# Performance work log

Measured on AMD Instinct MI355X. Metric: run time of the kernel, lower is better.

The kernel has to match this reference:

```python
import jax, jax.numpy as jnp
import numpy as np

M, N, C, D = 2, 8, 1024, 256  # n_routers, num_adapters, channel_dim, down_sample_size
B, S = 32, 512


def setup_inputs() -> dict:
    key = jax.random.key(0)
    k1, k2, k3, k4, k5 = jax.random.split(key, 5)
    x = jax.random.normal(k1, (B, S, C), dtype=jnp.float32)
    expert_index = jax.random.randint(k2, (M, B), 0, N, dtype=jnp.int32)
    down_w = jax.random.normal(k3, (M, N, C, D), dtype=jnp.float32) * 0.01
    down_b = jax.random.normal(k4, (M, N, D), dtype=jnp.float32) * 0.01
    up_w = jax.random.normal(k5, (M, N, D, C), dtype=jnp.float32) * 0.01
    return {"x": x, "expert_index": expert_index, "down_w": down_w,
            "down_b": down_b, "up_w": up_w}


def reference(x, expert_index, down_w, down_b, up_w):
    # Gather per-(router, batch-element) adapter weights along the adapter axis.
    idx = expert_index  # [M, B]
    bw_down = jnp.take_along_axis(down_w, idx[:, :, None, None], axis=1)  # [M, B, C, D]
    bb_down = jnp.take_along_axis(down_b, idx[:, :, None], axis=1)        # [M, B, D]
    bw_up = jnp.take_along_axis(up_w, idx[:, :, None, None], axis=1)      # [M, B, D, C]
    # z = swish(x @ W_down + b_down)  -> [M, B, S, D]
    z = jnp.einsum('bsc,mbcd->mbsd', x, bw_down) + bb_down[:, :, None, :]
    z = jax.nn.silu(z)
    # u = z @ W_up -> [M, B, S, C]
    u = jnp.einsum('mbsd,mbdc->mbsc', z, bw_up)
    return u
```

## Files before the change

### kernel.cpp

```cpp
#include <hip/hip_runtime.h>
#include <stdint.h>

typedef unsigned short u16;
typedef __bf16 bf16x8 __attribute__((ext_vector_type(8)));
typedef float f32x4 __attribute__((ext_vector_type(4)));

#define MM 2
#define NN 8
#define CC 1024
#define DD 256
#define BB 32
#define SS 512

__device__ __forceinline__ u16 f2bf(float f) {
  uint32_t u = __float_as_uint(f);
  u += 0x7FFFu + ((u >> 16) & 1u);
  return (u16)(u >> 16);
}

__device__ __forceinline__ uint32_t pack2(float a, float b) {
  return (uint32_t)f2bf(a) | ((uint32_t)f2bf(b) << 16);
}

__device__ __forceinline__ void async16(const void* g, void* l) {
  __builtin_amdgcn_global_load_lds(
      (const __attribute__((address_space(1))) uint32_t*)g,
      (__attribute__((address_space(3))) uint32_t*)l, 16, 0, 0);
}

__global__ __launch_bounds__(256) void prep_w(
    const float* __restrict__ dw, u16* __restrict__ wdT,
    const float* __restrict__ uw, u16* __restrict__ wuT,
    const float* __restrict__ x, u16* __restrict__ xb) {
  int bid = blockIdx.x;
  if (bid >= 4096) {
    const int t = bid - 4096;
    const float4* in4 = reinterpret_cast<const float4*>(x) + (size_t)t * 2048;
    uint2* out2 = reinterpret_cast<uint2*>(xb) + (size_t)t * 2048;
    const int tx = threadIdx.x;
#pragma unroll
    for (int k = 0; k < 8; ++k) {
      float4 v = in4[k * 256 + tx];
      out2[k * 256 + tx] = make_uint2(pack2(v.x, v.y), pack2(v.z, v.w));
    }
    return;
  }
  __shared__ float tile[64][33];
  const float* src; u16* dst; int K, N, tk, tn;
  if (bid < 2048) {
    K = CC; N = DD;
    const int slab = bid >> 7, t = bid & 127;
    tk = t >> 3; tn = t & 7;
    src = dw + (size_t)slab * K * N;
    dst = wdT + (size_t)slab * K * N;
  } else {
    bid -= 2048;
    K = DD; N = CC;
    const int slab = bid >> 7, t = bid & 127;
    tk = t >> 5; tn = t & 31;
    src = uw + (size_t)slab * K * N;
    dst = wuT + (size_t)slab * K * N;
  }
  const int k0 = tk * 64, n0 = tn * 32;
  const int tx = threadIdx.x & 31, ty = threadIdx.x >> 5;
#pragma unroll
  for (int i = 0; i < 64; i += 8)
    tile[ty + i][tx] = src[(size_t)(k0 + ty + i) * N + n0 + tx];
  __syncthreads();
  uint32_t* dst32 = reinterpret_cast<uint32_t*>(dst);
#pragma unroll
  for (int i = 0; i < 32; i += 8) {
    const int nr = ty + i;
    dst32[((size_t)(n0 + nr) * K + k0) / 2 + tx] =
        pack2(tile[2 * tx][nr], tile[2 * tx + 1][nr]);
  }
}

__global__ __launch_bounds__(512, 2) void fused_adapter(
    const u16* __restrict__ xb, const u16* __restrict__ wdT,
    const u16* __restrict__ wuT, const float* __restrict__ db,
    const int* __restrict__ eidx, float* __restrict__ out) {
  __shared__ __align__(16) u16 smA[2][128 * 64];
  __shared__ __align__(16) u16 smB[2][256 * 64];
  __shared__ __align__(16) u16 zl[8 * 128 * 32];

  const int id = blockIdx.x;
  const int xcd = id & 7;
  const int j5 = id >> 3;
  const int stile = j5 >> 3;
  const int m = (j5 >> 2) & 1;
  const int b = xcd * 4 + (j5 & 3);
  const int pair = m * BB + b;
  const int e = eidx[pair];
  const int s0 = stile * 128;

  const int tid = threadIdx.x;
  const int lane = tid & 63;
  const int wave = tid >> 6;
  const int quad = lane >> 4;
  const int l16 = lane & 15;
  const int fx = (l16 >> 1) & 3;
  const int fxr = l16 & 7;

  const int wr = (wave >> 2) * 64;
  const int wc = (wave & 3) * 64;

  const u16* Bd = wdT + (size_t)(m * NN + e) * DD * CC;
  const u16* Bu = wuT + (size_t)(m * NN + e) * CC * DD;

  const float* bias_p = db + (size_t)(m * NN + e) * DD;
  float biasr[4];
#pragma unroll
  for (int j = 0; j < 4; ++j) biasr[j] = bias_p[wc + j * 16 + l16];

  const int r_l = lane >> 3;
  const int sx = (lane & 7) ^ r_l;

  const u16* gA = xb + ((size_t)b * SS + s0 + wave * 16 + r_l) * CC + sx * 8;
  const u16* gBd = Bd + (size_t)(wave * 32 + r_l) * CC + sx * 8;
  const u16* gBu = Bu + (size_t)(wave * 32 + r_l) * DD + sx * 8;

  f32x4 acc[4][4];
#pragma unroll
  for (int i = 0; i < 4; ++i)
#pragma unroll
    for (int j = 0; j < 4; ++j) acc[i][j] = (f32x4){0.f, 0.f, 0.f, 0.f};

#pragma unroll
  for (int s = 0; s < 2; ++s)
    async16(gA + (size_t)(s * 8) * CC, &smA[0][(wave * 16 + s * 8) * 64]);
#pragma unroll
  for (int s = 0; s < 4; ++s)
    async16(gBd + (size_t)(s * 8) * CC, &smB[0][(wave * 32 + s * 8) * 64]);
  asm volatile("s_waitcnt vmcnt(0) lgkmcnt(0)" ::: "memory");
  __builtin_amdgcn_s_barrier();

  for (int kk = 0; kk < 16; ++kk) {
    const int cur = kk & 1, nxt = cur ^ 1;
    if (kk < 15) {
      const int ko = (kk + 1) * 64;
#pragma unroll
      for (int s = 0; s < 2; ++s)
        async16(gA + (size_t)(s * 8) * CC + ko, &smA[nxt][(wave * 16 + s * 8) * 64]);
#pragma unroll
      for (int s = 0; s < 4; ++s)
        async16(gBd + (size_t)(s * 8) * CC + ko, &smB[nxt][(wave * 32 + s * 8) * 64]);
    } else {
#pragma unroll
      for (int s = 0; s < 4; ++s)
        async16(gBu + (size_t)(s * 8) * DD, &smB[nxt][(wave * 32 + s * 8) * 64]);
    }
#pragma unroll
    for (int h = 0; h < 2; ++h) {
      bf16x8 af[4], bfr[4];
#pragma unroll
      for (int i = 0; i < 4; ++i)
        af[i] = *reinterpret_cast<const bf16x8*>(
            &smA[cur][(wr + i * 16 + l16) * 64 + ((h * 4 + quad) ^ fxr) * 8]);
#pragma unroll
      for (int j = 0; j < 4; ++j)
        bfr[j] = *reinterpret_cast<const bf16x8*>(
            &smB[cur][(wc + j * 16 + l16) * 64 + ((h * 4 + quad) ^ fxr) * 8]);
      __builtin_amdgcn_s_setprio(1);
#pragma unroll
      for (int i = 0; i < 4; ++i)
#pragma unroll
        for (int j = 0; j < 4; ++j)
          acc[i][j] = __builtin_amdgcn_mfma_f32_16x16x32_bf16(af[i], bfr[j], acc[i][j], 0, 0, 0);
      __builtin_amdgcn_s_setprio(0);
    }
    asm volatile("s_waitcnt vmcnt(0) lgkmcnt(0)" ::: "memory");
    __builtin_amdgcn_s_barrier();
  }

#pragma unroll
  for (int j = 0; j < 4; ++j) {
    const int d = wc + j * 16 + l16;
    const int kt = d >> 5;
    const int kl = d & 31;
    const int slot0 = kl >> 3;
    const int kin = kl & 7;
#pragma unroll
    for (int i = 0; i < 4; ++i) {
      const int zr = wr + i * 16 + quad * 4;
#pragma unroll
      for (int r = 0; r < 4; ++r) {
        const int row = zr + r;
        float v = acc[i][j][r] + biasr[j];
        v = v / (1.f + __expf(-v));
        zl[kt * 4096 + row * 32 + ((slot0 ^ ((row >> 1) & 3)) * 8) + kin] = f2bf(v);
      }
    }
  }
  asm volatile("s_waitcnt lgkmcnt(0)" ::: "memory");
  __builtin_amdgcn_s_barrier();

  float* ob = out + ((size_t)pair * SS + s0) * CC;

  for (int g = 0; g < 16; ++g) {
    const int cur2 = g & 1, nxt2 = cur2 ^ 1;
    const int ct = g >> 2;
    const int it2 = g & 3;
    if (g < 15) {
      const int g2 = g + 1;
      const size_t ro = (size_t)(g2 >> 2) * 256 * DD + (g2 & 3) * 64;
#pragma unroll
      for (int s = 0; s < 4; ++s)
        async16(gBu + ro + (size_t)(s * 8) * DD, &smB[nxt2][(wave * 32 + s * 8) * 64]);
    }
    if (it2 == 0) {
#pragma unroll
      for (int i = 0; i < 4; ++i)
#pragma unroll
        for (int j = 0; j < 4; ++j) acc[i][j] = (f32x4){0.f, 0.f, 0.f, 0.f};
    }
#pragma unroll
    for (int h = 0; h < 2; ++h) {
      bf16x8 af[4], bfr[4];
#pragma unroll
      for (int i = 0; i < 4; ++i)
        af[i] = *reinterpret_cast<const bf16x8*>(
            &zl[(it2 * 2 + h) * 4096 + (wr + i * 16 + l16) * 32 + (quad ^ fx) * 8]);
#pragma unroll
      for (int j = 0; j < 4; ++j)
        bfr[j] = *reinterpret_cast<const bf16x8*>(
            &smB[cur2][(wc + j * 16 + l16) * 64 + ((h * 4 + quad) ^ fxr) * 8]);
      __builtin_amdgcn_s_setprio(1);
#pragma unroll
      for (int i = 0; i < 4; ++i)
#pragma unroll
        for (int j = 0; j < 4; ++j)
          acc[i][j] = __builtin_amdgcn_mfma_f32_16x16x32_bf16(af[i], bfr[j], acc[i][j], 0, 0, 0);
      __builtin_amdgcn_s_setprio(0);
    }
    if (it2 == 3) {
#pragma unroll
      for (int j = 0; j < 4; ++j) {
        const int c = ct * 256 + wc + j * 16 + l16;
#pragma unroll
        for (int i = 0; i < 4; ++i) {
          const int sr = wr + i * 16 + quad * 4;
#pragma unroll
          for (int r = 0; r < 4; ++r)
            ob[(size_t)(sr + r) * CC + c] = acc[i][j][r];
        }
      }
    }
    if (g < 15) {
      asm volatile("s_waitcnt vmcnt(0) lgkmcnt(0)" ::: "memory");
      __builtin_amdgcn_s_barrier();
    }
  }
}

extern "C" void kernel_launch(void* const* d_in, const int* in_sizes, int n_in,
                              void* d_out, int out_size, void* d_ws, size_t ws_size,
                              hipStream_t stream) {
  const float* x  = (const float*)d_in[0];
  const int* eidx = (const int*)d_in[1];
  const float* dw = (const float*)d_in[2];
  const float* db = (const float*)d_in[3];
  const float* uw = (const float*)d_in[4];
  float* out = (float*)d_out;

  char* ws = (char*)d_ws;
  u16* wdT = (u16*)(ws);
  u16* wuT = (u16*)(ws + (size_t)8 * 1024 * 1024);
  u16* xbf = (u16*)(ws + (size_t)16 * 1024 * 1024);

  prep_w<<<dim3(6144), dim3(256), 0, stream>>>(dw, wdT, uw, wuT, x, xbf);
  fused_adapter<<<dim3(256), dim3(512), 0, stream>>>(
      xbf, wdT, wuT, db, eidx, out);
}
```

Baseline: 275.8 us.

## Split fused adapter into down and up GEMM kernels with bf16 z intermediate

Replaces the single fused kernel (256 blocks, 512 threads) with two kernels. The first converts fp32 x to bf16 inline while loading it and computes z over 128x128 tiles (512 blocks), writing bf16 z to workspace. The second computes the up projection over 128x128 output tiles (2048 blocks). This removes the separate x conversion pass and raises parallelism beyond the 256 fused blocks, at the cost of writing z to global memory and reading it back plus an extra launch.

```diff
diff --git a/kernel.cpp b/kernel.cpp
--- a/kernel.cpp
+++ b/kernel.cpp
@@ -30,22 +30,9 @@
 
 __global__ __launch_bounds__(256) void prep_w(
     const float* __restrict__ dw, u16* __restrict__ wdT,
-    const float* __restrict__ uw, u16* __restrict__ wuT,
-    const float* __restrict__ x, u16* __restrict__ xb) {
+    const float* __restrict__ uw, u16* __restrict__ wuT) {
+  __shared__ float tile[64][33];
   int bid = blockIdx.x;
-  if (bid >= 4096) {
-    const int t = bid - 4096;
-    const float4* in4 = reinterpret_cast<const float4*>(x) + (size_t)t * 2048;
-    uint2* out2 = reinterpret_cast<uint2*>(xb) + (size_t)t * 2048;
-    const int tx = threadIdx.x;
-#pragma unroll
-    for (int k = 0; k < 8; ++k) {
-      float4 v = in4[k * 256 + tx];
-      out2[k * 256 + tx] = make_uint2(pack2(v.x, v.y), pack2(v.z, v.w));
-    }
-    return;
-  }
-  __shared__ float tile[64][33];
   const float* src; u16* dst; int K, N, tk, tn;
   if (bid < 2048) {
     K = CC; N = DD;
@@ -76,49 +63,54 @@
   }
 }
 
-__global__ __launch_bounds__(512, 2) void fused_adapter(
-    const u16* __restrict__ xb, const u16* __restrict__ wdT,
-    const u16* __restrict__ wuT, const float* __restrict__ db,
-    const int* __restrict__ eidx, float* __restrict__ out) {
+__global__ __launch_bounds__(256, 2) void k1_down(
+    const float* __restrict__ x, const u16* __restrict__ wdT,
+    const float* __restrict__ db, const int* __restrict__ eidx,
+    u16* __restrict__ z) {
   __shared__ __align__(16) u16 smA[2][128 * 64];
-  __shared__ __align__(16) u16 smB[2][256 * 64];
-  __shared__ __align__(16) u16 zl[8 * 128 * 32];
+  __shared__ __align__(16) u16 smB[2][128 * 64];
 
   const int id = blockIdx.x;
   const int xcd = id & 7;
-  const int j5 = id >> 3;
-  const int stile = j5 >> 3;
-  const int m = (j5 >> 2) & 1;
-  const int b = xcd * 4 + (j5 & 3);
+  const int j6 = id >> 3;
+  const int b = xcd * 4 + (j6 & 3);
+  const int rest = j6 >> 2;
+  const int m = rest & 1;
+  const int stile = (rest >> 1) & 3;
+  const int dtile = rest >> 3;
   const int pair = m * BB + b;
   const int e = eidx[pair];
   const int s0 = stile * 128;
+  const int d0 = dtile * 128;
 
   const int tid = threadIdx.x;
   const int lane = tid & 63;
   const int wave = tid >> 6;
   const int quad = lane >> 4;
   const int l16 = lane & 15;
-  const int fx = (l16 >> 1) & 3;
   const int fxr = l16 & 7;
 
-  const int wr = (wave >> 2) * 64;
-  const int wc = (wave & 3) * 64;
-
-  const u16* Bd = wdT + (size_t)(m * NN + e) * DD * CC;
-  const u16* Bu = wuT + (size_t)(m * NN + e) * CC * DD;
-
-  const float* bias_p = db + (size_t)(m * NN + e) * DD;
+  const int wr = (wave >> 1) * 64;
+  const int wc = (wave & 1) * 64;
+
+  const u16* Bd = wdT + (size_t)(m * NN + e) * DD * CC + (size_t)d0 * CC;
+
+  const float* bias_p = db + (size_t)(m * NN + e) * DD + d0;
   float biasr[4];
 #pragma unroll
   for (int j = 0; j < 4; ++j) biasr[j] = bias_p[wc + j * 16 + l16];
+
+  const int arow = tid >> 1;
+  const int ac0 = (tid & 1) * 4;
+  const float* gAx = x + ((size_t)b * SS + s0 + arow) * CC + ac0 * 8;
+  int lAs[4];
+#pragma unroll
+  for (int c = 0; c < 4; ++c)
+    lAs[c] = arow * 64 + (((ac0 + c) ^ (arow & 7)) * 8);
 
   const int r_l = lane >> 3;
   const int sx = (lane & 7) ^ r_l;
-
-  const u16* gA = xb + ((size_t)b * SS + s0 + wave * 16 + r_l) * CC + sx * 8;
   const u16* gBd = Bd + (size_t)(wave * 32 + r_l) * CC + sx * 8;
-  const u16* gBu = Bu + (size_t)(wave * 32 + r_l) * DD + sx * 8;
 
   f32x4 acc[4][4];
 #pragma unroll
@@ -126,29 +118,40 @@
 #pragma unroll
     for (int j = 0; j < 4; ++j) acc[i][j] = (f32x4){0.f, 0.f, 0.f, 0.f};
 
-#pragma unroll
-  for (int s = 0; s < 2; ++s)
-    async16(gA + (size_t)(s * 8) * CC, &smA[0][(wave * 16 + s * 8) * 64]);
-#pragma unroll
-  for (int s = 0; s < 4; ++s)
-    async16(gBd + (size_t)(s * 8) * CC, &smB[0][(wave * 32 + s * 8) * 64]);
+  {
+    float4 a[8];
+#pragma unroll
+    for (int c = 0; c < 4; ++c) {
+      a[2 * c]     = *reinterpret_cast<const float4*>(gAx + c * 8);
+      a[2 * c + 1] = *reinterpret_cast<const float4*>(gAx + c * 8 + 4);
+    }
+#pragma unroll
+    for (int s = 0; s < 4; ++s)
+      async16(gBd + (size_t)(s * 8) * CC, &smB[0][(wave * 32 + s * 8) * 64]);
+#pragma unroll
+    for (int c = 0; c < 4; ++c)
+      *reinterpret_cast<uint4*>(&smA[0][lAs[c]]) =
+          make_uint4(pack2(a[2 * c].x, a[2 * c].y), pack2(a[2 * c].z, a[2 * c].w),
+                     pack2(a[2 * c + 1].x, a[2 * c + 1].y),
+                     pack2(a[2 * c + 1].z, a[2 * c + 1].w));
+  }
   asm volatile("s_waitcnt vmcnt(0) lgkmcnt(0)" ::: "memory");
   __builtin_amdgcn_s_barrier();
 
   for (int kk = 0; kk < 16; ++kk) {
     const int cur = kk & 1, nxt = cur ^ 1;
+    float4 a[8];
     if (kk < 15) {
+      const float* gA = gAx + (kk + 1) * 64;
+#pragma unroll
+      for (int c = 0; c < 4; ++c) {
+        a[2 * c]     = *reinterpret_cast<const float4*>(gA + c * 8);
+        a[2 * c + 1] = *reinterpret_cast<const float4*>(gA + c * 8 + 4);
+      }
       const int ko = (kk + 1) * 64;
-#pragma unroll
-      for (int s = 0; s < 2; ++s)
-        async16(gA + (size_t)(s * 8) * CC + ko, &smA[nxt][(wave * 16 + s * 8) * 64]);
 #pragma unroll
       for (int s = 0; s < 4; ++s)
         async16(gBd + (size_t)(s * 8) * CC + ko, &smB[nxt][(wave * 32 + s * 8) * 64]);
-    } else {
-#pragma unroll
-      for (int s = 0; s < 4; ++s)
-        async16(gBu + (size_t)(s * 8) * DD, &smB[nxt][(wave * 32 + s * 8) * 64]);
     }
 #pragma unroll
     for (int h = 0; h < 2; ++h) {
@@ -169,50 +172,106 @@
           acc[i][j] = __builtin_amdgcn_mfma_f32_16x16x32_bf16(af[i], bfr[j], acc[i][j], 0, 0, 0);
       __builtin_amdgcn_s_setprio(0);
     }
+    if (kk < 15) {
+#pragma unroll
+      for (int c = 0; c < 4; ++c)
+        *reinterpret_cast<uint4*>(&smA[nxt][lAs[c]]) =
+            make_uint4(pack2(a[2 * c].x, a[2 * c].y), pack2(a[2 * c].z, a[2 * c].w),
+                       pack2(a[2 * c + 1].x, a[2 * c + 1].y),
+                       pack2(a[2 * c + 1].z, a[2 * c + 1].w));
+    }
     asm volatile("s_waitcnt vmcnt(0) lgkmcnt(0)" ::: "memory");
     __builtin_amdgcn_s_barrier();
   }
 
+  u16* bounce = &smA[0][0];
 #pragma unroll
   for (int j = 0; j < 4; ++j) {
-    const int d = wc + j * 16 + l16;
-    const int kt = d >> 5;
-    const int kl = d & 31;
-    const int slot0 = kl >> 3;
-    const int kin = kl & 7;
 #pragma unroll
     for (int i = 0; i < 4; ++i) {
-      const int zr = wr + i * 16 + quad * 4;
 #pragma unroll
       for (int r = 0; r < 4; ++r) {
-        const int row = zr + r;
+        const int row = wr + i * 16 + quad * 4 + r;
+        const int dl = wc + j * 16 + l16;
         float v = acc[i][j][r] + biasr[j];
         v = v / (1.f + __expf(-v));
-        zl[kt * 4096 + row * 32 + ((slot0 ^ ((row >> 1) & 3)) * 8) + kin] = f2bf(v);
+        bounce[row * 128 + (((dl >> 3) ^ (row & 7)) * 8) + (dl & 7)] = f2bf(v);
       }
     }
   }
   asm volatile("s_waitcnt lgkmcnt(0)" ::: "memory");
   __builtin_amdgcn_s_barrier();
-
-  float* ob = out + ((size_t)pair * SS + s0) * CC;
-
-  for (int g = 0; g < 16; ++g) {
-    const int cur2 = g & 1, nxt2 = cur2 ^ 1;
-    const int ct = g >> 2;
-    const int it2 = g & 3;
-    if (g < 15) {
-      const int g2 = g + 1;
-      const size_t ro = (size_t)(g2 >> 2) * 256 * DD + (g2 & 3) * 64;
-#pragma unroll
-      for (int s = 0; s < 4; ++s)
-        async16(gBu + ro + (size_t)(s * 8) * DD, &smB[nxt2][(wave * 32 + s * 8) * 64]);
-    }
-    if (it2 == 0) {
-#pragma unroll
-      for (int i = 0; i < 4; ++i)
-#pragma unroll
-        for (int j = 0; j < 4; ++j) acc[i][j] = (f32x4){0.f, 0.f, 0.f, 0.f};
+  const int orow = tid >> 1, ohalf = tid & 1;
+  u16* gz = z + ((size_t)pair * SS + s0 + orow) * DD + d0 + ohalf * 64;
+#pragma unroll
+  for (int n = 0; n < 8; ++n) {
+    const int c = ohalf * 8 + n;
+    uint4 v = *reinterpret_cast<uint4*>(
+        &bounce[orow * 128 + ((c ^ (orow & 7)) * 8)]);
+    *reinterpret_cast<uint4*>(gz + n * 8) = v;
+  }
+}
+
+__global__ __launch_bounds__(256, 2) void k2_up(
+    const u16* __restrict__ z, const u16* __restrict__ wuT,
+    const int* __restrict__ eidx, float* __restrict__ out) {
+  __shared__ __align__(16) u16 smA[2][128 * 64];
+  __shared__ __align__(16) u16 smB[2][128 * 64];
+
+  const int id = blockIdx.x;
+  const int xcd = id & 7;
+  const int j8 = id >> 3;
+  const int b = xcd * 4 + (j8 & 3);
+  const int rest = j8 >> 2;
+  const int m = rest & 1;
+  const int stile = (rest >> 1) & 3;
+  const int ctile = rest >> 3;
+  const int pair = m * BB + b;
+  const int e = eidx[pair];
+  const int s0 = stile * 128;
+  const int c0 = ctile * 128;
+
+  const int tid = threadIdx.x;
+  const int lane = tid & 63;
+  const int wave = tid >> 6;
+  const int quad = lane >> 4;
+  const int l16 = lane & 15;
+  const int fxr = l16 & 7;
+
+  const int wr = (wave >> 1) * 64;
+  const int wc = (wave & 1) * 64;
+
+  const u16* Bu = wuT + (size_t)(m * NN + e) * CC * DD + (size_t)c0 * DD;
+
+  const int r_l = lane >> 3;
+  const int sx = (lane & 7) ^ r_l;
+  const u16* gA = z + ((size_t)pair * SS + s0 + wave * 32 + r_l) * DD + sx * 8;
+  const u16* gB = Bu + (size_t)(wave * 32 + r_l) * DD + sx * 8;
+
+  f32x4 acc[4][4];
+#pragma unroll
+  for (int i = 0; i < 4; ++i)
+#pragma unroll
+    for (int j = 0; j < 4; ++j) acc[i][j] = (f32x4){0.f, 0.f, 0.f, 0.f};
+
+#pragma unroll
+  for (int s = 0; s < 4; ++s) {
+    async16(gA + (size_t)(s * 8) * DD, &smA[0][(wave * 32 + s * 8) * 64]);
+    async16(gB + (size_t)(s * 8) * DD, &smB[0][(wave * 32 + s * 8) * 64]);
+  }
+  asm volatile("s_waitcnt vmcnt(0) lgkmcnt(0)" ::: "memory");
+  __builtin_amdgcn_s_barrier();
+
+#pragma unroll
+  for (int g = 0; g < 4; ++g) {
+    const int cur = g & 1, nxt = cur ^ 1;
+    if (g < 3) {
+      const int ko = (g + 1) * 64;
+#pragma unroll
+      for (int s = 0; s < 4; ++s) {
+        async16(gA + (size_t)(s * 8) * DD + ko, &smA[nxt][(wave * 32 + s * 8) * 64]);
+        async16(gB + (size_t)(s * 8) * DD + ko, &smB[nxt][(wave * 32 + s * 8) * 64]);
+      }
     }
 #pragma unroll
     for (int h = 0; h < 2; ++h) {
@@ -220,11 +279,11 @@
 #pragma unroll
       for (int i = 0; i < 4; ++i)
         af[i] = *reinterpret_cast<const bf16x8*>(
-            &zl[(it2 * 2 + h) * 4096 + (wr + i * 16 + l16) * 32 + (quad ^ fx) * 8]);
+            &smA[cur][(wr + i * 16 + l16) * 64 + ((h * 4 + quad) ^ fxr) * 8]);
 #pragma unroll
       for (int j = 0; j < 4; ++j)
         bfr[j] = *reinterpret_cast<const bf16x8*>(
-            &smB[cur2][(wc + j * 16 + l16) * 64 + ((h * 4 + quad) ^ fxr) * 8]);
+            &smB[cur][(wc + j * 16 + l16) * 64 + ((h * 4 + quad) ^ fxr) * 8]);
       __builtin_amdgcn_s_setprio(1);
 #pragma unroll
       for (int i = 0; i < 4; ++i)
@@ -233,22 +292,22 @@
           acc[i][j] = __builtin_amdgcn_mfma_f32_16x16x32_bf16(af[i], bfr[j], acc[i][j], 0, 0, 0);
       __builtin_amdgcn_s_setprio(0);
     }
-    if (it2 == 3) {
-#pragma unroll
-      for (int j = 0; j < 4; ++j) {
-        const int c = ct * 256 + wc + j * 16 + l16;
-#pragma unroll
-        for (int i = 0; i < 4; ++i) {
-          const int sr = wr + i * 16 + quad * 4;
-#pragma unroll
-          for (int r = 0; r < 4; ++r)
-            ob[(size_t)(sr + r) * CC + c] = acc[i][j][r];
-        }
-      }
-    }
-    if (g < 15) {
+    if (g < 3) {
       asm volatile("s_waitcnt vmcnt(0) lgkmcnt(0)" ::: "memory");
       __builtin_amdgcn_s_barrier();
+    }
+  }
+
+  float* ob = out + ((size_t)pair * SS + s0) * CC;
+#pragma unroll
+  for (int j = 0; j < 4; ++j) {
+    const int c = c0 + wc + j * 16 + l16;
+#pragma unroll
+    for (int i = 0; i < 4; ++i) {
+      const int sr = wr + i * 16 + quad * 4;
+#pragma unroll
+      for (int r = 0; r < 4; ++r)
+        ob[(size_t)(sr + r) * CC + c] = acc[i][j][r];
     }
   }
 }
@@ -266,9 +325,9 @@
   char* ws = (char*)d_ws;
   u16* wdT = (u16*)(ws);
   u16* wuT = (u16*)(ws + (size_t)8 * 1024 * 1024);
-  u16* xbf = (u16*)(ws + (size_t)16 * 1024 * 1024);
-
-  prep_w<<<dim3(6144), dim3(256), 0, stream>>>(dw, wdT, uw, wuT, x, xbf);
-  fused_adapter<<<dim3(256), dim3(512), 0, stream>>>(
-      xbf, wdT, wuT, db, eidx, out);
-}
+  u16* zbf = (u16*)(ws + (size_t)16 * 1024 * 1024);
+
+  prep_w<<<dim3(4096), dim3(256), 0, stream>>>(dw, wdT, uw, wuT);
+  k1_down<<<dim3(512), dim3(256), 0, stream>>>(x, wdT, db, eidx, zbf);
+  k2_up<<<dim3(2048), dim3(256), 0, stream>>>(zbf, wuT, eidx, out);
+}
```

Result: slower. 283.9 us (+2.9%).
